# Kernel optimization log

Measured on AMD Instinct MI355X. Metric: run time of the kernel, lower is better.

Reference implementation:

```python
import jax, jax.numpy as jnp
import numpy as np

N, F = 8192, 128
NEG_INF = -9e15
LEAKY_ALPHA = 0.2

def setup_inputs() -> dict:
    key = jax.random.key(0)
    k1, k2, k3, k4 = jax.random.split(key, 4)
    x = jax.random.normal(k1, (N, F), dtype=jnp.float32)
    h0 = jax.random.normal(k2, (N, F), dtype=jnp.float32)
    # sparse-ish binary adjacency (density ~0.005) with self-loops so every row has a neighbor
    adj = (jax.random.uniform(k3, (N, N)) < 0.005).astype(jnp.float32)
    diag = jnp.arange(N)
    adj = adj.at[diag, diag].set(1.0)
    # xavier_uniform-ish init for attention vector a [2F, 1]
    limit = float(np.sqrt(6.0 / (2 * F + 1)) * 1.414)
    a = jax.random.uniform(k4, (2 * F, 1), minval=-limit, maxval=limit, dtype=jnp.float32)
    temp = jnp.zeros((5,), dtype=jnp.float32)  # reset_parameters fills 0 -> coe = 0.5
    return {"x": x, "h0": h0, "adj": adj, "a": a, "temp": temp, "lamda": 1, "l": 1}


def reference(x, h0, adj, a, temp, lamda, l):
    # beta = log(lamda/l + 1) is computed in the original but never used in the output math.
    f = x.shape[1]
    # GAT-style scores: e[i,j] = leakyrelu(x_i.a1 + x_j.a2)
    feat_1 = x @ a[:f]          # [N, 1]
    feat_2 = x @ a[f:]          # [N, 1]
    e = jax.nn.leaky_relu(feat_1 + feat_2.T, negative_slope=LEAKY_ALPHA)  # [N, N]
    att = jnp.where(adj > 0, e, NEG_INF)
    U = jax.nn.softmax(att, axis=1)          # [N, N]
    prop_u = U @ x                           # [N, F]
    rowsum = jnp.sum(0.5 * U * U, axis=1)    # [N]  (sum of U*P, P = 0.5*U)
    coe = jax.nn.sigmoid(temp)
    # forward lifting
    xi = x * rowsum[:, None]
    feat_odd = prop_u - xi
    feat_even = x + prop_u - xi
    feat = coe[2] * feat_odd + (1.0 - coe[2]) * feat_even
    # inverse lifting
    prop_u2 = U @ feat
    odd = feat - prop_u2
    even = coe[3] * prop_u2 + odd * rowsum[:, None]
    feat_prime = coe[1] * even + (1.0 - coe[1]) * odd
    return 0.2 * feat_prime + 0.8 * h0
```

## Files before the change

### kernel.cpp

```cpp
#include <hip/hip_runtime.h>
#include <math.h>

#define NN 8192
#define FF 128
#define CAP 128

typedef float nfloat4 __attribute__((ext_vector_type(4)));
typedef float nfloat2 __attribute__((ext_vector_type(2)));

__device__ __forceinline__ unsigned short f2bf(float f) {
  unsigned u = __float_as_uint(f);
  return (unsigned short)((u + 0x7fffu + ((u >> 16) & 1u)) >> 16);
}

__global__ __launch_bounds__(256) void k_scores(const float* __restrict__ x,
                                                const float* __restrict__ a,
                                                float* __restrict__ f1,
                                                float* __restrict__ f2,
                                                unsigned* __restrict__ xb) {
  const int w = threadIdx.x >> 6;
  const int lane = threadIdx.x & 63;
  const int row = blockIdx.x * 4 + w;
  float2 v = ((const float2*)(x + (size_t)row * FF))[lane];
  float2 A1 = ((const float2*)a)[lane];
  float2 A2 = ((const float2*)(a + FF))[lane];
  float s1 = v.x * A1.x + v.y * A1.y;
  float s2 = v.x * A2.x + v.y * A2.y;
  #pragma unroll
  for (int off = 32; off > 0; off >>= 1) {
    s1 += __shfl_down(s1, off);
    s2 += __shfl_down(s2, off);
  }
  if (lane == 0) { f1[row] = s1; f2[row] = s2; }
  unsigned pk = (unsigned)f2bf(v.x) | ((unsigned)f2bf(v.y) << 16);
  xb[(row << 6) + lane] = pk;
}

__global__ __launch_bounds__(256, 4) void k_scanfwd(
    const float* __restrict__ adj, const float* __restrict__ x,
    const unsigned* __restrict__ xb,
    const float* __restrict__ f1g, const float* __restrict__ f2g,
    const float* __restrict__ temp,
    int* __restrict__ nnzg, int* __restrict__ colsg, float* __restrict__ valsg,
    float* __restrict__ rowsumg, float* __restrict__ featg,
    unsigned* __restrict__ featb) {
  const int w = threadIdx.x >> 6;
  const int lane = threadIdx.x & 63;
  const int row = blockIdx.x * 4 + w;

  __shared__ int   s_c[4][CAP];
  __shared__ float s_u[4][CAP];

  const nfloat4* arow = (const nfloat4*)(adj + (size_t)row * NN);
  const unsigned long long lt = (1ull << lane) - 1ull;
  int run = 0;
  #pragma unroll 8
  for (int it = 0; it < 32; ++it) {
    nfloat4 v = arow[it * 64 + lane];
    bool c0 = v.x > 0.f, c1 = v.y > 0.f, c2 = v.z > 0.f, c3 = v.w > 0.f;
    unsigned long long b0 = __ballot(c0), b1 = __ballot(c1),
                       b2 = __ballot(c2), b3 = __ballot(c3);
    int pos = run + __popcll(b0 & lt) + __popcll(b1 & lt) +
                    __popcll(b2 & lt) + __popcll(b3 & lt);
    int j0 = (it * 64 + lane) * 4;
    if (c0) { if (pos < CAP) s_c[w][pos] = j0;     pos++; }
    if (c1) { if (pos < CAP) s_c[w][pos] = j0 + 1; pos++; }
    if (c2) { if (pos < CAP) s_c[w][pos] = j0 + 2; pos++; }
    if (c3) { if (pos < CAP) s_c[w][pos] = j0 + 3; pos++; }
    run += __popcll(b0) + __popcll(b1) + __popcll(b2) + __popcll(b3);
  }
  const int cnt = run < CAP ? run : CAP;

  const float F1 = f1g[row];
  const int i0 = lane, i1 = lane + 64;
  int col0 = (i0 < cnt) ? s_c[w][i0] : 0;
  int col1 = (i1 < cnt) ? s_c[w][i1] : 0;
  float e0 = -INFINITY, e1 = -INFINITY;
  if (i0 < cnt) { float s = F1 + f2g[col0]; e0 = s > 0.f ? s : 0.2f * s; }
  if (i1 < cnt) { float s = F1 + f2g[col1]; e1 = s > 0.f ? s : 0.2f * s; }
  float mx = fmaxf(e0, e1);
  #pragma unroll
  for (int off = 32; off > 0; off >>= 1) mx = fmaxf(mx, __shfl_xor(mx, off));
  float p0 = (i0 < cnt) ? expf(e0 - mx) : 0.f;
  float p1 = (i1 < cnt) ? expf(e1 - mx) : 0.f;
  float sm = p0 + p1;
  #pragma unroll
  for (int off = 32; off > 0; off >>= 1) sm += __shfl_xor(sm, off);
  float inv = 1.f / sm;
  float u0 = p0 * inv, u1 = p1 * inv;
  float q = u0 * u0 + u1 * u1;
  #pragma unroll
  for (int off = 32; off > 0; off >>= 1) q += __shfl_xor(q, off);
  const float rs = 0.5f * q;

  if (i0 < cnt) { s_u[w][i0] = u0; colsg[(size_t)row * CAP + i0] = col0;
                  valsg[(size_t)row * CAP + i0] = u0; }
  if (i1 < cnt) { s_u[w][i1] = u1; colsg[(size_t)row * CAP + i1] = col1;
                  valsg[(size_t)row * CAP + i1] = u1; }
  if (lane == 0) { nnzg[row] = cnt; rowsumg[row] = rs; }

  float acc0 = 0.f, acc1 = 0.f;
  int k = 0;
  for (; k + 7 < cnt; k += 8) {
    int   c0 = s_c[w][k],   c1 = s_c[w][k+1], c2 = s_c[w][k+2], c3 = s_c[w][k+3];
    int   c4 = s_c[w][k+4], c5 = s_c[w][k+5], c6 = s_c[w][k+6], c7 = s_c[w][k+7];
    float w0 = s_u[w][k],   w1 = s_u[w][k+1], w2 = s_u[w][k+2], w3 = s_u[w][k+3];
    float w4 = s_u[w][k+4], w5 = s_u[w][k+5], w6 = s_u[w][k+6], w7 = s_u[w][k+7];
    unsigned g0 = xb[(c0 << 6) + lane], g1 = xb[(c1 << 6) + lane];
    unsigned g2 = xb[(c2 << 6) + lane], g3 = xb[(c3 << 6) + lane];
    unsigned g4 = xb[(c4 << 6) + lane], g5 = xb[(c5 << 6) + lane];
    unsigned g6 = xb[(c6 << 6) + lane], g7 = xb[(c7 << 6) + lane];
    acc0 += w0 * __uint_as_float(g0 << 16) + w1 * __uint_as_float(g1 << 16)
          + w2 * __uint_as_float(g2 << 16) + w3 * __uint_as_float(g3 << 16)
          + w4 * __uint_as_float(g4 << 16) + w5 * __uint_as_float(g5 << 16)
          + w6 * __uint_as_float(g6 << 16) + w7 * __uint_as_float(g7 << 16);
    acc1 += w0 * __uint_as_float(g0 & 0xffff0000u) + w1 * __uint_as_float(g1 & 0xffff0000u)
          + w2 * __uint_as_float(g2 & 0xffff0000u) + w3 * __uint_as_float(g3 & 0xffff0000u)
          + w4 * __uint_as_float(g4 & 0xffff0000u) + w5 * __uint_as_float(g5 & 0xffff0000u)
          + w6 * __uint_as_float(g6 & 0xffff0000u) + w7 * __uint_as_float(g7 & 0xffff0000u);
  }
  for (; k < cnt; ++k) {
    int c = s_c[w][k]; float u = s_u[w][k];
    unsigned g = xb[(c << 6) + lane];
    acc0 += u * __uint_as_float(g << 16);
    acc1 += u * __uint_as_float(g & 0xffff0000u);
  }

  const float coe2 = 1.f / (1.f + expf(-temp[2]));
  float2 xv = ((const float2*)(x + (size_t)row * FF))[lane];
  float ft0 = acc0 - xv.x * rs + (1.f - coe2) * xv.x;
  float ft1 = acc1 - xv.y * rs + (1.f - coe2) * xv.y;
  float2 ftv; ftv.x = ft0; ftv.y = ft1;
  ((float2*)featg)[(row << 6) + lane] = ftv;
  featb[(row << 6) + lane] = (unsigned)f2bf(ft0) | ((unsigned)f2bf(ft1) << 16);
}

__global__ __launch_bounds__(256, 4) void k_bwd(
    const float* __restrict__ featg, const unsigned* __restrict__ featb,
    const float* __restrict__ h0, const float* __restrict__ temp,
    const int* __restrict__ nnzg, const int* __restrict__ colsg,
    const float* __restrict__ valsg, const float* __restrict__ rowsumg,
    float* __restrict__ out) {
  const int w = threadIdx.x >> 6;
  const int lane = threadIdx.x & 63;
  const int row = blockIdx.x * 4 + w;

  __shared__ int   s_c[4][CAP];
  __shared__ float s_u[4][CAP];

  const int cnt = nnzg[row];
  const int* cg = colsg + (size_t)row * CAP;
  const float* vg = valsg + (size_t)row * CAP;
  const int i0 = lane, i1 = lane + 64;
  if (i0 < cnt) { s_c[w][i0] = cg[i0]; s_u[w][i0] = vg[i0]; }
  if (i1 < cnt) { s_c[w][i1] = cg[i1]; s_u[w][i1] = vg[i1]; }

  const float rs = rowsumg[row];
  float2 ft = ((const float2*)featg)[(row << 6) + lane];
  nfloat2 h = __builtin_nontemporal_load(((const nfloat2*)h0) + (row << 6) + lane);
  const float coe1 = 1.f / (1.f + expf(-temp[1]));
  const float coe3 = 1.f / (1.f + expf(-temp[3]));

  float acc0 = 0.f, acc1 = 0.f;
  int k = 0;
  for (; k + 7 < cnt; k += 8) {
    int   c0 = s_c[w][k],   c1 = s_c[w][k+1], c2 = s_c[w][k+2], c3 = s_c[w][k+3];
    int   c4 = s_c[w][k+4], c5 = s_c[w][k+5], c6 = s_c[w][k+6], c7 = s_c[w][k+7];
    float w0 = s_u[w][k],   w1 = s_u[w][k+1], w2 = s_u[w][k+2], w3 = s_u[w][k+3];
    float w4 = s_u[w][k+4], w5 = s_u[w][k+5], w6 = s_u[w][k+6], w7 = s_u[w][k+7];
    unsigned g0 = featb[(c0 << 6) + lane], g1 = featb[(c1 << 6) + lane];
    unsigned g2 = featb[(c2 << 6) + lane], g3 = featb[(c3 << 6) + lane];
    unsigned g4 = featb[(c4 << 6) + lane], g5 = featb[(c5 << 6) + lane];
    unsigned g6 = featb[(c6 << 6) + lane], g7 = featb[(c7 << 6) + lane];
    acc0 += w0 * __uint_as_float(g0 << 16) + w1 * __uint_as_float(g1 << 16)
          + w2 * __uint_as_float(g2 << 16) + w3 * __uint_as_float(g3 << 16)
          + w4 * __uint_as_float(g4 << 16) + w5 * __uint_as_float(g5 << 16)
          + w6 * __uint_as_float(g6 << 16) + w7 * __uint_as_float(g7 << 16);
    acc1 += w0 * __uint_as_float(g0 & 0xffff0000u) + w1 * __uint_as_float(g1 & 0xffff0000u)
          + w2 * __uint_as_float(g2 & 0xffff0000u) + w3 * __uint_as_float(g3 & 0xffff0000u)
          + w4 * __uint_as_float(g4 & 0xffff0000u) + w5 * __uint_as_float(g5 & 0xffff0000u)
          + w6 * __uint_as_float(g6 & 0xffff0000u) + w7 * __uint_as_float(g7 & 0xffff0000u);
  }
  for (; k < cnt; ++k) {
    int c = s_c[w][k]; float u = s_u[w][k];
    unsigned g = featb[(c << 6) + lane];
    acc0 += u * __uint_as_float(g << 16);
    acc1 += u * __uint_as_float(g & 0xffff0000u);
  }

  float odd0 = ft.x - acc0, odd1 = ft.y - acc1;
  float ev0 = coe3 * acc0 + odd0 * rs;
  float ev1 = coe3 * acc1 + odd1 * rs;
  float fp0 = coe1 * ev0 + (1.f - coe1) * odd0;
  float fp1 = coe1 * ev1 + (1.f - coe1) * odd1;
  nfloat2 o;
  o.x = 0.2f * fp0 + 0.8f * h.x;
  o.y = 0.2f * fp1 + 0.8f * h.y;
  __builtin_nontemporal_store(o, ((nfloat2*)out) + (row << 6) + lane);
}

extern "C" void kernel_launch(void* const* d_in, const int* in_sizes, int n_in,
                              void* d_out, int out_size, void* d_ws, size_t ws_size,
                              hipStream_t stream) {
  const float* x    = (const float*)d_in[0];
  const float* h0   = (const float*)d_in[1];
  const float* adj  = (const float*)d_in[2];
  const float* a    = (const float*)d_in[3];
  const float* temp = (const float*)d_in[4];
  float* out = (float*)d_out;

  float* f1 = (float*)d_ws;
  float* f2 = f1 + NN;
  float* rowsum = f2 + NN;
  int*   nnz = (int*)(rowsum + NN);
  int*   cols = nnz + NN;
  float* vals = (float*)(cols + (size_t)NN * CAP);
  float* feat = vals + (size_t)NN * CAP;
  unsigned* xb = (unsigned*)(feat + (size_t)NN * FF);
  unsigned* featb = xb + (size_t)NN * 64;

  k_scores<<<NN / 4, 256, 0, stream>>>(x, a, f1, f2, xb);
  k_scanfwd<<<NN / 4, 256, 0, stream>>>(adj, x, xb, f1, f2, temp, nnz, cols, vals, rowsum, feat, featb);
  k_bwd<<<NN / 4, 256, 0, stream>>>(feat, featb, h0, temp, nnz, cols, vals, rowsum, out);
}
```

Baseline: 72.54 us.

## Process two rows per wave, overlapping next row's adjacency scan with current gather

New measurement: 79.52 us. 9.6% more time.

```diff
diff --git a/kernel.cpp b/kernel.cpp
--- a/kernel.cpp
+++ b/kernel.cpp
@@ -32,11 +32,10 @@
     s2 += __shfl_down(s2, off);
   }
   if (lane == 0) { f1[row] = s1; f2[row] = s2; }
-  unsigned pk = (unsigned)f2bf(v.x) | ((unsigned)f2bf(v.y) << 16);
-  xb[(row << 6) + lane] = pk;
-}
-
-__global__ __launch_bounds__(256, 4) void k_scanfwd(
+  xb[(row << 6) + lane] = (unsigned)f2bf(v.x) | ((unsigned)f2bf(v.y) << 16);
+}
+
+__global__ __launch_bounds__(256, 4) void k_scanfwd2(
     const float* __restrict__ adj, const float* __restrict__ x,
     const unsigned* __restrict__ xb,
     const float* __restrict__ f1g, const float* __restrict__ f2g,
@@ -46,66 +45,179 @@
     unsigned* __restrict__ featb) {
   const int w = threadIdx.x >> 6;
   const int lane = threadIdx.x & 63;
-  const int row = blockIdx.x * 4 + w;
-
-  __shared__ int   s_c[4][CAP];
-  __shared__ float s_u[4][CAP];
-
-  const nfloat4* arow = (const nfloat4*)(adj + (size_t)row * NN);
+  const int rowA = blockIdx.x * 8 + w * 2;
+  const int rowB = rowA + 1;
+  const int slA = w * 2, slB = slA + 1;
+
+  __shared__ int   s_c[8][CAP];
+  __shared__ float s_u[8][CAP];
+
   const unsigned long long lt = (1ull << lane) - 1ull;
-  int run = 0;
+  const nfloat4* arowA = (const nfloat4*)(adj + (size_t)rowA * NN);
+  const nfloat4* arowB = (const nfloat4*)(adj + (size_t)rowB * NN);
+  const float coe2 = 1.f / (1.f + expf(-temp[2]));
+
+  int runA = 0;
   #pragma unroll 8
   for (int it = 0; it < 32; ++it) {
-    nfloat4 v = arow[it * 64 + lane];
+    nfloat4 v = arowA[it * 64 + lane];
     bool c0 = v.x > 0.f, c1 = v.y > 0.f, c2 = v.z > 0.f, c3 = v.w > 0.f;
     unsigned long long b0 = __ballot(c0), b1 = __ballot(c1),
                        b2 = __ballot(c2), b3 = __ballot(c3);
-    int pos = run + __popcll(b0 & lt) + __popcll(b1 & lt) +
-                    __popcll(b2 & lt) + __popcll(b3 & lt);
+    int pos = runA + __popcll(b0 & lt) + __popcll(b1 & lt) +
+                     __popcll(b2 & lt) + __popcll(b3 & lt);
     int j0 = (it * 64 + lane) * 4;
-    if (c0) { if (pos < CAP) s_c[w][pos] = j0;     pos++; }
-    if (c1) { if (pos < CAP) s_c[w][pos] = j0 + 1; pos++; }
-    if (c2) { if (pos < CAP) s_c[w][pos] = j0 + 2; pos++; }
-    if (c3) { if (pos < CAP) s_c[w][pos] = j0 + 3; pos++; }
-    run += __popcll(b0) + __popcll(b1) + __popcll(b2) + __popcll(b3);
-  }
-  const int cnt = run < CAP ? run : CAP;
-
-  const float F1 = f1g[row];
-  const int i0 = lane, i1 = lane + 64;
-  int col0 = (i0 < cnt) ? s_c[w][i0] : 0;
-  int col1 = (i1 < cnt) ? s_c[w][i1] : 0;
-  float e0 = -INFINITY, e1 = -INFINITY;
-  if (i0 < cnt) { float s = F1 + f2g[col0]; e0 = s > 0.f ? s : 0.2f * s; }
-  if (i1 < cnt) { float s = F1 + f2g[col1]; e1 = s > 0.f ? s : 0.2f * s; }
-  float mx = fmaxf(e0, e1);
-  #pragma unroll
-  for (int off = 32; off > 0; off >>= 1) mx = fmaxf(mx, __shfl_xor(mx, off));
-  float p0 = (i0 < cnt) ? expf(e0 - mx) : 0.f;
-  float p1 = (i1 < cnt) ? expf(e1 - mx) : 0.f;
-  float sm = p0 + p1;
-  #pragma unroll
-  for (int off = 32; off > 0; off >>= 1) sm += __shfl_xor(sm, off);
-  float inv = 1.f / sm;
-  float u0 = p0 * inv, u1 = p1 * inv;
-  float q = u0 * u0 + u1 * u1;
-  #pragma unroll
-  for (int off = 32; off > 0; off >>= 1) q += __shfl_xor(q, off);
-  const float rs = 0.5f * q;
-
-  if (i0 < cnt) { s_u[w][i0] = u0; colsg[(size_t)row * CAP + i0] = col0;
-                  valsg[(size_t)row * CAP + i0] = u0; }
-  if (i1 < cnt) { s_u[w][i1] = u1; colsg[(size_t)row * CAP + i1] = col1;
-                  valsg[(size_t)row * CAP + i1] = u1; }
-  if (lane == 0) { nnzg[row] = cnt; rowsumg[row] = rs; }
+    if (c0) { if (pos < CAP) s_c[slA][pos] = j0;     pos++; }
+    if (c1) { if (pos < CAP) s_c[slA][pos] = j0 + 1; pos++; }
+    if (c2) { if (pos < CAP) s_c[slA][pos] = j0 + 2; pos++; }
+    if (c3) { if (pos < CAP) s_c[slA][pos] = j0 + 3; pos++; }
+    runA += __popcll(b0) + __popcll(b1) + __popcll(b2) + __popcll(b3);
+  }
+  const int cntA = runA < CAP ? runA : CAP;
+
+  nfloat4 bb[8];
+  int runB = 0;
+  float accA0 = 0.f, accA1 = 0.f;
+  int ka = 0;
+
+#define LOAD_CHUNK(base) { _Pragma("unroll") \
+    for (int i = 0; i < 8; ++i) bb[i] = arowB[((base) + i) * 64 + lane]; }
+
+#define PROC_CHUNK(base) { _Pragma("unroll") \
+    for (int i = 0; i < 8; ++i) { \
+      nfloat4 v = bb[i]; \
+      bool c0 = v.x > 0.f, c1 = v.y > 0.f, c2 = v.z > 0.f, c3 = v.w > 0.f; \
+      unsigned long long b0 = __ballot(c0), b1 = __ballot(c1), \
+                         b2 = __ballot(c2), b3 = __ballot(c3); \
+      int pos = runB + __popcll(b0 & lt) + __popcll(b1 & lt) + \
+                       __popcll(b2 & lt) + __popcll(b3 & lt); \
+      int j0 = (((base) + i) * 64 + lane) * 4; \
+      if (c0) { if (pos < CAP) s_c[slB][pos] = j0;     pos++; } \
+      if (c1) { if (pos < CAP) s_c[slB][pos] = j0 + 1; pos++; } \
+      if (c2) { if (pos < CAP) s_c[slB][pos] = j0 + 2; pos++; } \
+      if (c3) { if (pos < CAP) s_c[slB][pos] = j0 + 3; pos++; } \
+      runB += __popcll(b0) + __popcll(b1) + __popcll(b2) + __popcll(b3); } }
+
+#define ROUND_A_BODY { \
+      int   c0 = s_c[slA][ka],   c1 = s_c[slA][ka+1], c2 = s_c[slA][ka+2], c3 = s_c[slA][ka+3]; \
+      int   c4 = s_c[slA][ka+4], c5 = s_c[slA][ka+5], c6 = s_c[slA][ka+6], c7 = s_c[slA][ka+7]; \
+      float w0 = s_u[slA][ka],   w1 = s_u[slA][ka+1], w2 = s_u[slA][ka+2], w3 = s_u[slA][ka+3]; \
+      float w4 = s_u[slA][ka+4], w5 = s_u[slA][ka+5], w6 = s_u[slA][ka+6], w7 = s_u[slA][ka+7]; \
+      unsigned g0 = xb[(c0 << 6) + lane], g1 = xb[(c1 << 6) + lane]; \
+      unsigned g2 = xb[(c2 << 6) + lane], g3 = xb[(c3 << 6) + lane]; \
+      unsigned g4 = xb[(c4 << 6) + lane], g5 = xb[(c5 << 6) + lane]; \
+      unsigned g6 = xb[(c6 << 6) + lane], g7 = xb[(c7 << 6) + lane]; \
+      accA0 += w0 * __uint_as_float(g0 << 16) + w1 * __uint_as_float(g1 << 16) \
+             + w2 * __uint_as_float(g2 << 16) + w3 * __uint_as_float(g3 << 16) \
+             + w4 * __uint_as_float(g4 << 16) + w5 * __uint_as_float(g5 << 16) \
+             + w6 * __uint_as_float(g6 << 16) + w7 * __uint_as_float(g7 << 16); \
+      accA1 += w0 * __uint_as_float(g0 & 0xffff0000u) + w1 * __uint_as_float(g1 & 0xffff0000u) \
+             + w2 * __uint_as_float(g2 & 0xffff0000u) + w3 * __uint_as_float(g3 & 0xffff0000u) \
+             + w4 * __uint_as_float(g4 & 0xffff0000u) + w5 * __uint_as_float(g5 & 0xffff0000u) \
+             + w6 * __uint_as_float(g6 & 0xffff0000u) + w7 * __uint_as_float(g7 & 0xffff0000u); \
+      ka += 8; }
+
+  LOAD_CHUNK(0);
+
+  float rsA;
+  {
+    const float F1 = f1g[rowA];
+    const int i0 = lane, i1 = lane + 64;
+    int col0 = (i0 < cntA) ? s_c[slA][i0] : 0;
+    int col1 = (i1 < cntA) ? s_c[slA][i1] : 0;
+    float e0 = -INFINITY, e1 = -INFINITY;
+    if (i0 < cntA) { float s = F1 + f2g[col0]; e0 = s > 0.f ? s : 0.2f * s; }
+    if (i1 < cntA) { float s = F1 + f2g[col1]; e1 = s > 0.f ? s : 0.2f * s; }
+    float mx = fmaxf(e0, e1);
+    #pragma unroll
+    for (int off = 32; off > 0; off >>= 1) mx = fmaxf(mx, __shfl_xor(mx, off));
+    float p0 = (i0 < cntA) ? expf(e0 - mx) : 0.f;
+    float p1 = (i1 < cntA) ? expf(e1 - mx) : 0.f;
+    float sm = p0 + p1;
+    #pragma unroll
+    for (int off = 32; off > 0; off >>= 1) sm += __shfl_xor(sm, off);
+    float inv = 1.f / sm;
+    float u0 = p0 * inv, u1 = p1 * inv;
+    float q = u0 * u0 + u1 * u1;
+    #pragma unroll
+    for (int off = 32; off > 0; off >>= 1) q += __shfl_xor(q, off);
+    rsA = 0.5f * q;
+    if (i0 < cntA) { s_u[slA][i0] = u0; colsg[(size_t)rowA * CAP + i0] = col0;
+                     valsg[(size_t)rowA * CAP + i0] = u0; }
+    if (i1 < cntA) { s_u[slA][i1] = u1; colsg[(size_t)rowA * CAP + i1] = col1;
+                     valsg[(size_t)rowA * CAP + i1] = u1; }
+    if (lane == 0) { nnzg[rowA] = cntA; rowsumg[rowA] = rsA; }
+  }
+
+  PROC_CHUNK(0);
+  LOAD_CHUNK(8);
+  if (ka + 7 < cntA) ROUND_A_BODY;
+  if (ka + 7 < cntA) ROUND_A_BODY;
+  PROC_CHUNK(8);
+  LOAD_CHUNK(16);
+  if (ka + 7 < cntA) ROUND_A_BODY;
+  if (ka + 7 < cntA) ROUND_A_BODY;
+  PROC_CHUNK(16);
+  LOAD_CHUNK(24);
+  if (ka + 7 < cntA) ROUND_A_BODY;
+  if (ka + 7 < cntA) ROUND_A_BODY;
+  PROC_CHUNK(24);
+  const int cntB = runB < CAP ? runB : CAP;
+
+  while (ka + 7 < cntA) ROUND_A_BODY;
+  for (; ka < cntA; ++ka) {
+    int c = s_c[slA][ka]; float u = s_u[slA][ka];
+    unsigned g = xb[(c << 6) + lane];
+    accA0 += u * __uint_as_float(g << 16);
+    accA1 += u * __uint_as_float(g & 0xffff0000u);
+  }
+
+  {
+    float2 xv = ((const float2*)x)[(rowA << 6) + lane];
+    float f0 = accA0 - xv.x * rsA + (1.f - coe2) * xv.x;
+    float f1v = accA1 - xv.y * rsA + (1.f - coe2) * xv.y;
+    float2 fv; fv.x = f0; fv.y = f1v;
+    ((float2*)featg)[(rowA << 6) + lane] = fv;
+    featb[(rowA << 6) + lane] = (unsigned)f2bf(f0) | ((unsigned)f2bf(f1v) << 16);
+  }
+
+  float rsB;
+  {
+    const float F1 = f1g[rowB];
+    const int i0 = lane, i1 = lane + 64;
+    int col0 = (i0 < cntB) ? s_c[slB][i0] : 0;
+    int col1 = (i1 < cntB) ? s_c[slB][i1] : 0;
+    float e0 = -INFINITY, e1 = -INFINITY;
+    if (i0 < cntB) { float s = F1 + f2g[col0]; e0 = s > 0.f ? s : 0.2f * s; }
+    if (i1 < cntB) { float s = F1 + f2g[col1]; e1 = s > 0.f ? s : 0.2f * s; }
+    float mx = fmaxf(e0, e1);
+    #pragma unroll
+    for (int off = 32; off > 0; off >>= 1) mx = fmaxf(mx, __shfl_xor(mx, off));
+    float p0 = (i0 < cntB) ? expf(e0 - mx) : 0.f;
+    float p1 = (i1 < cntB) ? expf(e1 - mx) : 0.f;
+    float sm = p0 + p1;
+    #pragma unroll
+    for (int off = 32; off > 0; off >>= 1) sm += __shfl_xor(sm, off);
+    float inv = 1.f / sm;
+    float u0 = p0 * inv, u1 = p1 * inv;
+    float q = u0 * u0 + u1 * u1;
+    #pragma unroll
+    for (int off = 32; off > 0; off >>= 1) q += __shfl_xor(q, off);
+    rsB = 0.5f * q;
+    if (i0 < cntB) { s_u[slB][i0] = u0; colsg[(size_t)rowB * CAP + i0] = col0;
+                     valsg[(size_t)rowB * CAP + i0] = u0; }
+    if (i1 < cntB) { s_u[slB][i1] = u1; colsg[(size_t)rowB * CAP + i1] = col1;
+                     valsg[(size_t)rowB * CAP + i1] = u1; }
+    if (lane == 0) { nnzg[rowB] = cntB; rowsumg[rowB] = rsB; }
+  }
 
   float acc0 = 0.f, acc1 = 0.f;
   int k = 0;
-  for (; k + 7 < cnt; k += 8) {
-    int   c0 = s_c[w][k],   c1 = s_c[w][k+1], c2 = s_c[w][k+2], c3 = s_c[w][k+3];
-    int   c4 = s_c[w][k+4], c5 = s_c[w][k+5], c6 = s_c[w][k+6], c7 = s_c[w][k+7];
-    float w0 = s_u[w][k],   w1 = s_u[w][k+1], w2 = s_u[w][k+2], w3 = s_u[w][k+3];
-    float w4 = s_u[w][k+4], w5 = s_u[w][k+5], w6 = s_u[w][k+6], w7 = s_u[w][k+7];
+  for (; k + 7 < cntB; k += 8) {
+    int   c0 = s_c[slB][k],   c1 = s_c[slB][k+1], c2 = s_c[slB][k+2], c3 = s_c[slB][k+3];
+    int   c4 = s_c[slB][k+4], c5 = s_c[slB][k+5], c6 = s_c[slB][k+6], c7 = s_c[slB][k+7];
+    float w0 = s_u[slB][k],   w1 = s_u[slB][k+1], w2 = s_u[slB][k+2], w3 = s_u[slB][k+3];
+    float w4 = s_u[slB][k+4], w5 = s_u[slB][k+5], w6 = s_u[slB][k+6], w7 = s_u[slB][k+7];
     unsigned g0 = xb[(c0 << 6) + lane], g1 = xb[(c1 << 6) + lane];
     unsigned g2 = xb[(c2 << 6) + lane], g3 = xb[(c3 << 6) + lane];
     unsigned g4 = xb[(c4 << 6) + lane], g5 = xb[(c5 << 6) + lane];
@@ -119,20 +231,23 @@
           + w4 * __uint_as_float(g4 & 0xffff0000u) + w5 * __uint_as_float(g5 & 0xffff0000u)
           + w6 * __uint_as_float(g6 & 0xffff0000u) + w7 * __uint_as_float(g7 & 0xffff0000u);
   }
-  for (; k < cnt; ++k) {
-    int c = s_c[w][k]; float u = s_u[w][k];
+  for (; k < cntB; ++k) {
+    int c = s_c[slB][k]; float u = s_u[slB][k];
     unsigned g = xb[(c << 6) + lane];
     acc0 += u * __uint_as_float(g << 16);
     acc1 += u * __uint_as_float(g & 0xffff0000u);
   }
-
-  const float coe2 = 1.f / (1.f + expf(-temp[2]));
-  float2 xv = ((const float2*)(x + (size_t)row * FF))[lane];
-  float ft0 = acc0 - xv.x * rs + (1.f - coe2) * xv.x;
-  float ft1 = acc1 - xv.y * rs + (1.f - coe2) * xv.y;
-  float2 ftv; ftv.x = ft0; ftv.y = ft1;
-  ((float2*)featg)[(row << 6) + lane] = ftv;
-  featb[(row << 6) + lane] = (unsigned)f2bf(ft0) | ((unsigned)f2bf(ft1) << 16);
+  {
+    float2 xv = ((const float2*)x)[(rowB << 6) + lane];
+    float f0 = acc0 - xv.x * rsB + (1.f - coe2) * xv.x;
+    float f1v = acc1 - xv.y * rsB + (1.f - coe2) * xv.y;
+    float2 fv; fv.x = f0; fv.y = f1v;
+    ((float2*)featg)[(rowB << 6) + lane] = fv;
+    featb[(rowB << 6) + lane] = (unsigned)f2bf(f0) | ((unsigned)f2bf(f1v) << 16);
+  }
+#undef LOAD_CHUNK
+#undef PROC_CHUNK
+#undef ROUND_A_BODY
 }
 
 __global__ __launch_bounds__(256, 4) void k_bwd(
@@ -220,6 +335,6 @@
   unsigned* featb = xb + (size_t)NN * 64;
 
   k_scores<<<NN / 4, 256, 0, stream>>>(x, a, f1, f2, xb);
-  k_scanfwd<<<NN / 4, 256, 0, stream>>>(adj, x, xb, f1, f2, temp, nnz, cols, vals, rowsum, feat, featb);
+  k_scanfwd2<<<NN / 8, 256, 0, stream>>>(adj, x, xb, f1, f2, temp, nnz, cols, vals, rowsum, feat, featb);
   k_bwd<<<NN / 4, 256, 0, stream>>>(feat, featb, h0, temp, nnz, cols, vals, rowsum, out);
 }
```
